# Performance work log

Measured on AMD Instinct MI355X. Metric: run time of the kernel, lower is better.

The kernel has to match this reference:

```python
import jax, jax.numpy as jnp
import numpy as np


def setup_inputs() -> dict:
    key = jax.random.key(0)
    k1, k2 = jax.random.split(key)
    B, N = 32, 2048
    preds = jax.random.normal(k1, (B, N), dtype=jnp.float32)
    targets = jax.random.uniform(k2, (B, N), dtype=jnp.float32)
    return {"preds": preds, "targets": targets}


def reference(preds, targets):
    B, N = preds.shape
    # sort preds descending, permute targets accordingly
    idx = jnp.argsort(-preds, axis=1)                      # [B, N]
    sorted_preds = jnp.take_along_axis(preds, idx, axis=1)
    sorted_targets = jnp.take_along_axis(targets, idx, axis=1)

    # pairwise score diffs and sigmoid loss: [B, N, N]
    diffs = sorted_preds[:, :, None] - sorted_preds[:, None, :]
    pairwise_loss = jax.nn.sigmoid(-diffs)

    # delta-NDCG: |(t_i - t_j) * (log2(rank_j + 2) - log2(rank_i + 2))|
    # ranks are 1..N (constants, detached in original)
    ranks = jnp.arange(1, N + 1, dtype=jnp.float32)
    disc = jnp.log2(ranks + 2.0)                            # [N]
    discount_diff = disc[None, :] - disc[:, None]           # [i, j] -> disc_j - disc_i
    gain_diff = sorted_targets[:, :, None] - sorted_targets[:, None, :]
    deltas = jnp.abs(gain_diff * discount_diff[None, :, :]) # [B, N, N]

    loss = jnp.sum(pairwise_loss * deltas) / B
    return loss
```

## Files before the change

kernel.cpp:

```cpp
#include <hip/hip_runtime.h>

#define BN 2048
#define BB 32
#define NPAIRBLK (2 * 32 * 8)


__global__ __launch_bounds__(256) void rank_disc_kernel(const float* __restrict__ preds,
                                                        float* __restrict__ disc) {
    __shared__ float sp[BN];
    const int row = blockIdx.y;
    const float* prow = preds + row * BN;

    for (int i = threadIdx.x; i < BN / 4; i += 256) {
        ((float4*)sp)[i] = ((const float4*)prow)[i];
    }
    __syncthreads();

    const int plocal = threadIdx.x >> 3;
    const int qoct   = threadIdx.x & 7;
    const int p = blockIdx.x * 32 + plocal;
    const float pp = sp[p];

    int cnt = 0;
    for (int f = qoct; f < BN / 4; f += 8) {
        float4 v = ((const float4*)sp)[f];
        cnt += (v.x > pp);
        cnt += (v.y > pp);
        cnt += (v.z > pp);
        cnt += (v.w > pp);
    }
    cnt += __shfl_xor(cnt, 1, 64);
    cnt += __shfl_xor(cnt, 2, 64);
    cnt += __shfl_xor(cnt, 4, 64);
    if (qoct == 0) {
        disc[row * BN + p] = log2f((float)(cnt + 3));
    }
}

__global__ __launch_bounds__(256) void pair_sum_kernel(const float* __restrict__ targets,
                                                       const float* __restrict__ disc,
                                                       float* __restrict__ partials) {
    __shared__ float st[256];
    __shared__ float sd[256];
    const int row = blockIdx.y;
    const float* trow = targets + row * BN;
    const float* drow = disc + row * BN;
    const int qbase = blockIdx.z * 256;

    st[threadIdx.x] = trow[qbase + threadIdx.x];
    sd[threadIdx.x] = drow[qbase + threadIdx.x];
    __syncthreads();

    const int pbase = blockIdx.x * 1024 + threadIdx.x;
    float tp[4], dp[4], acc[4];
    #pragma unroll
    for (int k = 0; k < 4; k++) {
        tp[k] = trow[pbase + k * 256];
        dp[k] = drow[pbase + k * 256];
        acc[k] = 0.0f;
    }

    for (int q = 0; q < 256; q += 4) {
        float4 tv = ((const float4*)st)[q >> 2];
        float4 dv = ((const float4*)sd)[q >> 2];
        #pragma unroll
        for (int k = 0; k < 4; k++) {
            acc[k] += fabsf(tp[k] - tv.x) * fabsf(dp[k] - dv.x);
            acc[k] += fabsf(tp[k] - tv.y) * fabsf(dp[k] - dv.y);
            acc[k] += fabsf(tp[k] - tv.z) * fabsf(dp[k] - dv.z);
            acc[k] += fabsf(tp[k] - tv.w) * fabsf(dp[k] - dv.w);
        }
    }
    float a = (acc[0] + acc[1]) + (acc[2] + acc[3]);

    for (int off = 32; off > 0; off >>= 1) a += __shfl_down(a, off, 64);
    __shared__ float warp_acc[4];
    if ((threadIdx.x & 63) == 0) warp_acc[threadIdx.x >> 6] = a;
    __syncthreads();
    if (threadIdx.x == 0) {
        const int bid = (blockIdx.z * gridDim.y + blockIdx.y) * gridDim.x + blockIdx.x;
        partials[bid] = warp_acc[0] + warp_acc[1] + warp_acc[2] + warp_acc[3];
    }
}

__global__ __launch_bounds__(256) void finalize_kernel(const float* __restrict__ partials,
                                                       float* __restrict__ out) {
    float acc = partials[threadIdx.x] + partials[threadIdx.x + 256];
    for (int off = 32; off > 0; off >>= 1) acc += __shfl_down(acc, off, 64);
    __shared__ float warp_acc[4];
    if ((threadIdx.x & 63) == 0) warp_acc[threadIdx.x >> 6] = acc;
    __syncthreads();
    if (threadIdx.x == 0) {
        out[0] = (warp_acc[0] + warp_acc[1] + warp_acc[2] + warp_acc[3])
                 * (1.0f / (2.0f * BB));
    }
}

extern "C" void kernel_launch(void* const* d_in, const int* in_sizes, int n_in,
                              void* d_out, int out_size, void* d_ws, size_t ws_size,
                              hipStream_t stream) {
    const float* preds = (const float*)d_in[0];
    const float* targets = (const float*)d_in[1];
    float* out = (float*)d_out;
    float* disc = (float*)d_ws;
    float* partials = (float*)d_ws + BB * BN;

    dim3 gridA(BN / 32, BB);
    rank_disc_kernel<<<gridA, 256, 0, stream>>>(preds, disc);

    dim3 gridB(2, BB, BN / 256);
    pair_sum_kernel<<<gridB, 256, 0, stream>>>(targets, disc, partials);

    finalize_kernel<<<1, 256, 0, stream>>>(partials, out);
}
```

Measured before the change: 84.24 us.

## Register-block rank counting and pair sum over more elements per thread

The rank kernel now has each thread compare every loaded float4 from shared memory against 8 pivot values instead of 1, so blocks cover 128 positions and the final disc values are written as float4s. The pair-sum kernel is retiled: each thread holds 8 row elements, blocks take 128-column tiles, and the grid becomes 16x32, still 512 partials. This raises arithmetic per shared-memory load and cuts the number of blocks, in exchange for higher register pressure and fewer blocks to spread across the GPU.

```diff
diff --git a/kernel.cpp b/kernel.cpp
--- a/kernel.cpp
+++ b/kernel.cpp
@@ -2,7 +2,7 @@
 
 #define BN 2048
 #define BB 32
-#define NPAIRBLK (2 * 32 * 8)
+#define NPAIRBLK (32 * 16)
 
 
 __global__ __launch_bounds__(256) void rank_disc_kernel(const float* __restrict__ preds,
@@ -16,70 +16,87 @@
     }
     __syncthreads();
 
-    const int plocal = threadIdx.x >> 3;
-    const int qoct   = threadIdx.x & 7;
-    const int p = blockIdx.x * 32 + plocal;
-    const float pp = sp[p];
+    const int c = threadIdx.x >> 4;
+    const int s = threadIdx.x & 15;
+    const int pbase = blockIdx.x * 128 + c * 8;
 
-    int cnt = 0;
-    for (int f = qoct; f < BN / 4; f += 8) {
+    float pp[8];
+    #pragma unroll
+    for (int k = 0; k < 8; k++) pp[k] = sp[pbase + k];
+
+    int cnt[8] = {0, 0, 0, 0, 0, 0, 0, 0};
+    for (int f = s; f < BN / 4; f += 16) {
         float4 v = ((const float4*)sp)[f];
-        cnt += (v.x > pp);
-        cnt += (v.y > pp);
-        cnt += (v.z > pp);
-        cnt += (v.w > pp);
+        #pragma unroll
+        for (int k = 0; k < 8; k++) {
+            cnt[k] += (v.x > pp[k]);
+            cnt[k] += (v.y > pp[k]);
+            cnt[k] += (v.z > pp[k]);
+            cnt[k] += (v.w > pp[k]);
+        }
     }
-    cnt += __shfl_xor(cnt, 1, 64);
-    cnt += __shfl_xor(cnt, 2, 64);
-    cnt += __shfl_xor(cnt, 4, 64);
-    if (qoct == 0) {
-        disc[row * BN + p] = log2f((float)(cnt + 3));
+    #pragma unroll
+    for (int k = 0; k < 8; k++) {
+        cnt[k] += __shfl_xor(cnt[k], 1, 64);
+        cnt[k] += __shfl_xor(cnt[k], 2, 64);
+        cnt[k] += __shfl_xor(cnt[k], 4, 64);
+        cnt[k] += __shfl_xor(cnt[k], 8, 64);
+    }
+    if (s == 0) {
+        float o[8];
+        #pragma unroll
+        for (int k = 0; k < 8; k++) o[k] = log2f((float)(cnt[k] + 3));
+        float4* dst = (float4*)(disc + row * BN + pbase);
+        dst[0] = make_float4(o[0], o[1], o[2], o[3]);
+        dst[1] = make_float4(o[4], o[5], o[6], o[7]);
     }
 }
 
 __global__ __launch_bounds__(256) void pair_sum_kernel(const float* __restrict__ targets,
                                                        const float* __restrict__ disc,
                                                        float* __restrict__ partials) {
-    __shared__ float st[256];
-    __shared__ float sd[256];
+    __shared__ float st[128];
+    __shared__ float sd[128];
     const int row = blockIdx.y;
     const float* trow = targets + row * BN;
     const float* drow = disc + row * BN;
-    const int qbase = blockIdx.z * 256;
+    const int qbase = blockIdx.x * 128;
 
-    st[threadIdx.x] = trow[qbase + threadIdx.x];
-    sd[threadIdx.x] = drow[qbase + threadIdx.x];
+    if (threadIdx.x < 128) {
+        st[threadIdx.x] = trow[qbase + threadIdx.x];
+        sd[threadIdx.x] = drow[qbase + threadIdx.x];
+    }
     __syncthreads();
 
-    const int pbase = blockIdx.x * 1024 + threadIdx.x;
-    float tp[4], dp[4], acc[4];
+    float tp[8], dp[8], acc[8];
     #pragma unroll
-    for (int k = 0; k < 4; k++) {
-        tp[k] = trow[pbase + k * 256];
-        dp[k] = drow[pbase + k * 256];
+    for (int k = 0; k < 8; k++) {
+        tp[k] = trow[threadIdx.x + k * 256];
+        dp[k] = drow[threadIdx.x + k * 256];
         acc[k] = 0.0f;
     }
 
-    for (int q = 0; q < 256; q += 4) {
+    for (int q = 0; q < 128; q += 4) {
         float4 tv = ((const float4*)st)[q >> 2];
         float4 dv = ((const float4*)sd)[q >> 2];
         #pragma unroll
-        for (int k = 0; k < 4; k++) {
+        for (int k = 0; k < 8; k++) {
             acc[k] += fabsf(tp[k] - tv.x) * fabsf(dp[k] - dv.x);
             acc[k] += fabsf(tp[k] - tv.y) * fabsf(dp[k] - dv.y);
             acc[k] += fabsf(tp[k] - tv.z) * fabsf(dp[k] - dv.z);
             acc[k] += fabsf(tp[k] - tv.w) * fabsf(dp[k] - dv.w);
         }
     }
-    float a = (acc[0] + acc[1]) + (acc[2] + acc[3]);
+    float a = ((acc[0] + acc[1]) + (acc[2] + acc[3]))
+            + ((acc[4] + acc[5]) + (acc[6] + acc[7]));
 
     for (int off = 32; off > 0; off >>= 1) a += __shfl_down(a, off, 64);
     __shared__ float warp_acc[4];
     if ((threadIdx.x & 63) == 0) warp_acc[threadIdx.x >> 6] = a;
     __syncthreads();
     if (threadIdx.x == 0) {
-        const int bid = (blockIdx.z * gridDim.y + blockIdx.y) * gridDim.x + blockIdx.x;
-        partials[bid] = warp_acc[0] + warp_acc[1] + warp_acc[2] + warp_acc[3];
+        partials[blockIdx.y * gridDim.x + blockIdx.x] =
+            warp_acc[0] + warp_acc[1] + warp_acc[2] + warp_acc[3];
     }
 }
 
@@ -105,10 +122,10 @@
     float* disc = (float*)d_ws;
     float* partials = (float*)d_ws + BB * BN;
 
-    dim3 gridA(BN / 32, BB);
+    dim3 gridA(BN / 128, BB);
     rank_disc_kernel<<<gridA, 256, 0, stream>>>(preds, disc);
 
-    dim3 gridB(2, BB, BN / 256);
+    dim3 gridB(BN / 128, BB);
     pair_sum_kernel<<<gridB, 256, 0, stream>>>(targets, disc, partials);
 
     finalize_kernel<<<1, 256, 0, stream>>>(partials, out);
```

Result: no change. 83.76 us (-0.6%).
